# Kernel tuning notes

Hardware: AMD Instinct MI355X
Metric: run time of the kernel (lower is better)

## Reference

```python
import jax, jax.numpy as jnp
import numpy as np

HEAD_DIM = 64

def setup_inputs() -> dict:
    key = jax.random.key(0)
    ks = jax.random.split(key, 6)
    b, q_len, kv_len, emb, h, d = 4, 2048, 2048, 1024, 16, HEAD_DIM
    scale = 1.0 / np.sqrt(emb)  # fan_in variance scaling for stable logits
    return {
        "inputs_q": jax.random.normal(ks[0], (b, q_len, emb), jnp.float32),
        "inputs_kv": jax.random.normal(ks[1], (b, kv_len, emb), jnp.float32),
        "Wq": jax.random.normal(ks[2], (emb, h, d), jnp.float32) * scale,
        "Wk": jax.random.normal(ks[3], (emb, h, d), jnp.float32) * scale,
        "Wv": jax.random.normal(ks[4], (emb, h, d), jnp.float32) * scale,
        "Wo": jax.random.normal(ks[5], (h, d, emb), jnp.float32) * scale,
    }

def reference(inputs_q, inputs_kv, Wq, Wk, Wv, Wo):
    # QKV projections; query kernel init includes 1/sqrt(head_dim) in the
    depth_scale = jnp.sqrt(jnp.asarray(HEAD_DIM, inputs_q.dtype))
    q = jnp.einsum('bqe,ehd->bqhd', inputs_q, Wq) / depth_scale
    k = jnp.einsum('bke,ehd->bkhd', inputs_kv, Wk)
    v = jnp.einsum('bke,ehd->bkhd', inputs_kv, Wv)
    # full attention: einsum -> softmax -> einsum (naive, materializes bhqk)
    attn_weights = jnp.einsum('bqhd,bkhd->bhqk', q, k)
    attn_weights = jax.nn.softmax(attn_weights, axis=-1)
    out = jnp.einsum('bhqk,bkhd->bqhd', attn_weights, v)
    # output projection over (heads, head_dim)
    return jnp.einsum('bqhd,hde->bqe', out, Wo)
```

## Files before the change

### kernel.cpp

```cpp
#include <hip/hip_runtime.h>
#include <hip/hip_bf16.h>


typedef __attribute__((ext_vector_type(8))) short bf16x8;
typedef __attribute__((ext_vector_type(2))) float f32x2;
typedef __attribute__((ext_vector_type(4))) float f32x4;
typedef __attribute__((ext_vector_type(16))) float f32x16;

#define MFMA16(a, b, c) __builtin_amdgcn_mfma_f32_16x16x32_bf16((a), (b), (c), 0, 0, 0)
#define MFMA32(a, b, c) __builtin_amdgcn_mfma_f32_32x32x16_bf16((a), (b), (c), 0, 0, 0)

__device__ __forceinline__ short f2bf(float f) {
  union { float f; unsigned u; } v; v.f = f;
  unsigned r = v.u + 0x7fffu + ((v.u >> 16) & 1u);
  return (short)(r >> 16);
}

__device__ __forceinline__ unsigned cvtpk(float lo, float hi) {
  unsigned r;
  asm("v_cvt_pk_bf16_f32 %0, %1, %2" : "=v"(r) : "v"(lo), "v"(hi));
  return r;
}

__device__ __forceinline__ void plswap(unsigned& a, unsigned& b) {
  asm volatile("v_permlane32_swap_b32 %0, %1" : "+v"(a), "+v"(b));
}

#if __has_builtin(__builtin_amdgcn_permlane32_swap)
typedef __attribute__((ext_vector_type(2))) unsigned u32x2;
__device__ __forceinline__ float xhalf_max(float x) {
  float y = x;
  asm("" : "+v"(y));
  const u32x2 r = __builtin_amdgcn_permlane32_swap(
      __float_as_uint(x), __float_as_uint(y), false, false);
  return fmaxf(__uint_as_float(r[0]), __uint_as_float(r[1]));
}
__device__ __forceinline__ float xhalf_add(float x) {
  float y = x;
  asm("" : "+v"(y));
  const u32x2 r = __builtin_amdgcn_permlane32_swap(
      __float_as_uint(x), __float_as_uint(y), false, false);
  return __uint_as_float(r[0]) + __uint_as_float(r[1]);
}
#else
__device__ __forceinline__ float xhalf_max(float x) {
  float a, b;
  asm volatile(
      "v_mov_b32 %0, %2\n\t"
      "v_mov_b32 %1, %2\n\t"
      "s_nop 2\n\t"
      "v_permlane32_swap_b32 %0, %1"
      : "=&v"(a), "=&v"(b)
      : "v"(x));
  return fmaxf(a, b);
}
__device__ __forceinline__ float xhalf_add(float x) {
  float a, b;
  asm volatile(
      "v_mov_b32 %0, %2\n\t"
      "v_mov_b32 %1, %2\n\t"
      "s_nop 2\n\t"
      "v_permlane32_swap_b32 %0, %1"
      : "=&v"(a), "=&v"(b)
      : "v"(x));
  return a + b;
}
#endif

__device__ __forceinline__ void gld16(const short* g, short* l) {
  __builtin_amdgcn_global_load_lds(
      (const __attribute__((address_space(1))) unsigned int*)g,
      (__attribute__((address_space(3))) unsigned int*)l, 16, 0, 0);
}

__global__ __launch_bounds__(256) void cast_kernel(
    const float* __restrict__ in, short* __restrict__ out, int n8) {
  int i = blockIdx.x * 256 + threadIdx.x;
  const int stride = gridDim.x * 256;
  for (; i < n8; i += stride) {
    const float4 f0 = ((const float4*)in)[2 * i];
    const float4 f1 = ((const float4*)in)[2 * i + 1];
    bf16x8 v;
    v[0] = f2bf(f0.x); v[1] = f2bf(f0.y); v[2] = f2bf(f0.z); v[3] = f2bf(f0.w);
    v[4] = f2bf(f1.x); v[5] = f2bf(f1.y); v[6] = f2bf(f1.z); v[7] = f2bf(f1.w);
    ((bf16x8*)out)[i] = v;
  }
}

__global__ __launch_bounds__(256) void wtrans_kernel(
    const float* __restrict__ w0, const float* __restrict__ w1,
    const float* __restrict__ w2, const float* __restrict__ w3,
    short* __restrict__ out) {
  __shared__ float t[32][33];
  const int z = blockIdx.z;
  const float* src = (z == 0) ? w0 : (z == 1) ? w1 : (z == 2) ? w2 : w3;
  short* dst = out + (size_t)z * (1024 * 1024);
  const int x = threadIdx.x & 31, y = threadIdx.x >> 5;
  const int n0 = blockIdx.x * 32, k0 = blockIdx.y * 32;
#pragma unroll
  for (int yy = y; yy < 32; yy += 8)
    t[yy][x] = src[(size_t)(k0 + yy) * 1024 + n0 + x];
  __syncthreads();
#pragma unroll
  for (int yy = y; yy < 32; yy += 8)
    dst[(size_t)(n0 + yy) * 1024 + k0 + x] = f2bf(t[x][yy]);
}

template <bool OUTF32, bool SWZ>
__global__ __launch_bounds__(256) void gemm_bb(
    const short* __restrict__ A, const short* __restrict__ B,
    void* __restrict__ Cp, int M, int N, int K, int ldc, float scale) {
  __shared__ __align__(16) short At[128][64];
  __shared__ __align__(16) short Bt[128][64];
  const int tid = threadIdx.x, l = tid & 63, w = tid >> 6;
  const int wm = (w >> 1) * 64, wn = (w & 1) * 64;
  int bx = blockIdx.x, by = blockIdx.y;
  if (SWZ) {
    const int nbx = gridDim.x;
    const int lin = by * nbx + bx;
    const int cpx = (nbx * gridDim.y) >> 3;
    const int swz = (lin & 7) * cpx + (lin >> 3);
    bx = swz % nbx;
    by = swz / nbx;
  }
  const int m0 = by * 128, n0 = bx * 128;
  const short* Abase = A + (size_t)(m0 + w * 8 + (l >> 3)) * K + (l & 7) * 8;
  const short* Bbase = B + (size_t)(n0 + w * 8 + (l >> 3)) * K + (l & 7) * 8;

  f32x4 acc[4][4];
#pragma unroll
  for (int i = 0; i < 4; ++i)
#pragma unroll
    for (int j = 0; j < 4; ++j) acc[i][j] = (f32x4){0.f, 0.f, 0.f, 0.f};

  for (int k0 = 0; k0 < K; k0 += 64) {
    __syncthreads();
#pragma unroll
    for (int i = 0; i < 4; ++i) {
      gld16(Abase + (size_t)i * 32 * K + k0, &At[i * 32 + w * 8][0]);
      gld16(Bbase + (size_t)i * 32 * K + k0, &Bt[i * 32 + w * 8][0]);
    }
    __syncthreads();
#pragma unroll
    for (int ks = 0; ks < 2; ++ks) {
      bf16x8 af[4], bfr[4];
#pragma unroll
      for (int mt = 0; mt < 4; ++mt)
        af[mt] = *(const bf16x8*)&At[wm + mt * 16 + (l & 15)][ks * 32 + (l >> 4) * 8];
#pragma unroll
      for (int nt = 0; nt < 4; ++nt)
        bfr[nt] = *(const bf16x8*)&Bt[wn + nt * 16 + (l & 15)][ks * 32 + (l >> 4) * 8];
#pragma unroll
      for (int mt = 0; mt < 4; ++mt)
#pragma unroll
        for (int nt = 0; nt < 4; ++nt)
          acc[mt][nt] = MFMA16(af[mt], bfr[nt], acc[mt][nt]);
    }
  }
#pragma unroll
  for (int mt = 0; mt < 4; ++mt)
#pragma unroll
    for (int nt = 0; nt < 4; ++nt)
#pragma unroll
      for (int r = 0; r < 4; ++r) {
        const int row = m0 + wm + mt * 16 + (l >> 4) * 4 + r;
        const int col = n0 + wn + nt * 16 + (l & 15);
        const float v = acc[mt][nt][r] * scale;
        if (OUTF32)
          ((float*)Cp)[(size_t)row * ldc + col] = v;
        else
          ((short*)Cp)[(size_t)row * ldc + col] = f2bf(v);
      }
}

__global__ __launch_bounds__(512) void attn8w_kernel(
    const short* __restrict__ qb, const short* __restrict__ kb,
    const short* __restrict__ vT, short* __restrict__ ob) {
  __shared__ __align__(16) short Ksh[2][64][64];
  __shared__ __align__(16) short Vsh[2][64][64];
  const int tid = threadIdx.x, w = tid >> 6, l = tid & 63;
  const int hi = l >> 5, ln = l & 31;
  const int lin = blockIdx.y * 8 + blockIdx.x;
  const int swz = (lin & 7) * 64 + (lin >> 3);
  const int qc = swz & 7, bh = swz >> 3;
  const int b = bh >> 4, h = bh & 15;
  const size_t bL = (size_t)b * 2048;
  const int hd = h * 64;
  const int q0 = qc * 256 + w * 32;

  const int sr0 = w * 8 + (l >> 3);
  const int sc0 = ((l & 7) ^ (sr0 & 7)) << 3;

#define STAGE(BUF, KV0)                                                    \
  do {                                                                     \
    gld16(kb + (bL + (KV0) + sr0) * 1024 + hd + sc0, &Ksh[BUF][w * 8][0]); \
    gld16(vT + (size_t)(hd + sr0) * 8192 + bL + (KV0) + sc0,               \
          &Vsh[BUF][w * 8][0]);                                            \
  } while (0)

  bf16x8 qf[4];
  {
    const short* qrow = qb + (bL + q0 + ln) * 1024 + hd + hi * 8;
#pragma unroll
    for (int c = 0; c < 4; ++c) qf[c] = *(const bf16x8*)(qrow + c * 16);
  }

  f32x16 o0, o1;
#pragma unroll
  for (int i = 0; i < 16; ++i) { o0[i] = 0.f; o1[i] = 0.f; }
  float m = -1e30f, lsum = 0.f;

  const int swzk = ln & 7;

  STAGE(0, 0);
  int cur = 0;
  for (int t = 0; t < 32; ++t) {
    __syncthreads();
    if (t < 31) STAGE(cur ^ 1, (t + 1) * 64);

    f32x16 s0, s1;
#pragma unroll
    for (int i = 0; i < 16; ++i) { s0[i] = 0.f; s1[i] = 0.f; }
    __builtin_amdgcn_s_setprio(1);
#pragma unroll
    for (int c = 0; c < 4; ++c) {
      const int bcol = ((((c << 1) | hi)) ^ swzk) << 3;
      const bf16x8 kf0 = *(const bf16x8*)&Ksh[cur][ln][bcol];
      const bf16x8 kf1 = *(const bf16x8*)&Ksh[cur][32 + ln][bcol];
      s0 = MFMA32(kf0, qf[c], s0);
      s1 = MFMA32(kf1, qf[c], s1);
    }
    __builtin_amdgcn_s_setprio(0);

    f32x2 pm0 = (f32x2){s0[0], s0[1]};
    f32x2 pm1 = (f32x2){s1[0], s1[1]};
#pragma unroll
    for (int i = 1; i < 8; ++i) {
      pm0 = __builtin_elementwise_max(pm0, (f32x2){s0[2 * i], s0[2 * i + 1]});
      pm1 = __builtin_elementwise_max(pm1, (f32x2){s1[2 * i], s1[2 * i + 1]});
    }
    pm0 = __builtin_elementwise_max(pm0, pm1);
    float pmax = fmaxf(pm0[0], pm0[1]);
    pmax = xhalf_max(pmax);

    if (!__all(pmax - m <= 8.0f)) {
      const float mnew = fmaxf(m, pmax);
      const float fac = exp2f(m - mnew);
      m = mnew;
      lsum *= fac;
      o0 *= fac;
      o1 *= fac;
    }

    float p0[16], p1[16];
    const f32x2 m2 = (f32x2){m, m};
    f32x2 acc2 = (f32x2){0.f, 0.f};
#pragma unroll
    for (int i = 0; i < 8; ++i) {
      const f32x2 d0 = (f32x2){s0[2 * i], s0[2 * i + 1]} - m2;
      const f32x2 d1 = (f32x2){s1[2 * i], s1[2 * i + 1]} - m2;
      p0[2 * i] = exp2f(d0[0]);
      p0[2 * i + 1] = exp2f(d0[1]);
      p1[2 * i] = exp2f(d1[0]);
      p1[2 * i + 1] = exp2f(d1[1]);
      acc2 += (f32x2){p0[2 * i], p0[2 * i + 1]};
      acc2 += (f32x2){p1[2 * i], p1[2 * i + 1]};
    }
    lsum += acc2[0] + acc2[1];

    __builtin_amdgcn_s_setprio(1);
#define PVCHUNK(PARR, BASE, C)                                               \
  do {                                                                       \
    unsigned A0 = cvtpk(PARR[(BASE) + 0], PARR[(BASE) + 1]);                 \
    unsigned A1 = cvtpk(PARR[(BASE) + 2], PARR[(BASE) + 3]);                 \
    unsigned B0 = cvtpk(PARR[(BASE) + 4], PARR[(BASE) + 5]);                 \
    unsigned B1 = cvtpk(PARR[(BASE) + 6], PARR[(BASE) + 7]);                 \
    plswap(A0, B0);                                                          \
    plswap(A1, B1);                                                          \
    union { unsigned u[4]; bf16x8 v; } pf;                                   \
    pf.u[0] = A0; pf.u[1] = A1; pf.u[2] = B0; pf.u[3] = B1;                  \
    const int bcol = ((((C) << 1) | hi) ^ swzk) << 3;                        \
    const bf16x8 vf0 = *(const bf16x8*)&Vsh[cur][ln][bcol];                  \
    const bf16x8 vf1 = *(const bf16x8*)&Vsh[cur][32 + ln][bcol];             \
    o0 = MFMA32(vf0, pf.v, o0);                                              \
    o1 = MFMA32(vf1, pf.v, o1);                                              \
  } while (0)

    PVCHUNK(p0, 0, 0);
    PVCHUNK(p0, 8, 1);
    PVCHUNK(p1, 0, 2);
    PVCHUNK(p1, 8, 3);
#undef PVCHUNK
    __builtin_amdgcn_s_setprio(0);

    cur ^= 1;
  }

  const float inv = 1.0f / xhalf_add(lsum);
  short* orow = ob + (bL + q0 + ln) * 1024 + hd + hi * 4;
#pragma unroll
  for (int g = 0; g < 4; ++g) {
    const unsigned a0 = cvtpk(o0[4 * g + 0] * inv, o0[4 * g + 1] * inv);
    const unsigned a1 = cvtpk(o0[4 * g + 2] * inv, o0[4 * g + 3] * inv);
    *(uint2*)(orow + 8 * g) = make_uint2(a0, a1);
    const unsigned b0 = cvtpk(o1[4 * g + 0] * inv, o1[4 * g + 1] * inv);
    const unsigned b1 = cvtpk(o1[4 * g + 2] * inv, o1[4 * g + 3] * inv);
    *(uint2*)(orow + 32 + 8 * g) = make_uint2(b0, b1);
  }
#undef STAGE
}

extern "C" void kernel_launch(void* const* d_in, const int* in_sizes, int n_in,
                              void* d_out, int out_size, void* d_ws,
                              size_t ws_size, hipStream_t stream) {
  const size_t ML = (size_t)8192 * 1024;
  short* qb = (short*)d_ws;
  short* kb = qb + ML;
  short* vT = kb + ML;
  short* ob = vT + ML;
  short* wT = ob + ML;
  short* WqT = wT;
  short* WkT = wT + (size_t)1024 * 1024;
  short* WvT = wT + (size_t)2 * 1024 * 1024;
  short* WoT = wT + (size_t)3 * 1024 * 1024;
  short* qibf = vT;
  short* kvbf = ob;

  wtrans_kernel<<<dim3(32, 32, 4), 256, 0, stream>>>(
      (const float*)d_in[2], (const float*)d_in[3], (const float*)d_in[4],
      (const float*)d_in[5], wT);

  cast_kernel<<<2048, 256, 0, stream>>>((const float*)d_in[0], qibf,
                                        (int)(ML / 8));
  cast_kernel<<<2048, 256, 0, stream>>>((const float*)d_in[1], kvbf,
                                        (int)(ML / 8));

  gemm_bb<false, true><<<dim3(8, 64), 256, 0, stream>>>(
      qibf, WqT, qb, 8192, 1024, 1024, 1024, 0.125f * 1.44269504f);
  gemm_bb<false, true><<<dim3(8, 64), 256, 0, stream>>>(
      kvbf, WkT, kb, 8192, 1024, 1024, 1024, 1.0f);
  gemm_bb<false, false><<<dim3(64, 8), 256, 0, stream>>>(
      WvT, kvbf, vT, 1024, 8192, 1024, 8192, 1.0f);

  attn8w_kernel<<<dim3(8, 64), 512, 0, stream>>>(qb, kb, vT, ob);

  gemm_bb<true, true><<<dim3(8, 64), 256, 0, stream>>>(
      ob, WoT, d_out, 8192, 1024, 1024, 1024, 1.0f);
}
```

Baseline: 249.3 us.

## Software-pipeline QK and softmax/PV in attention, merge Q/K projection GEMMs

The attention loop is restructured so the QK^T MFMAs for the next KV tile are issued before the softmax and PV of the previous tile. K stays double-buffered, V moves to a triple buffer, and there are two sets of score registers. The Q and K projection GEMMs are merged into a single launch with a swizzled 3D grid, which cuts one launch and fills the device better. Launch bounds now request 4 waves per SIMD. The extra score registers and the occupancy hint may cause spills, and the extra LDS may limit occupancy.

```diff
diff --git a/kernel.cpp b/kernel.cpp
--- a/kernel.cpp
+++ b/kernel.cpp
@@ -46,23 +46,17 @@
 __device__ __forceinline__ float xhalf_max(float x) {
   float a, b;
   asm volatile(
-      "v_mov_b32 %0, %2\n\t"
-      "v_mov_b32 %1, %2\n\t"
-      "s_nop 2\n\t"
+      "v_mov_b32 %0, %2\n\tv_mov_b32 %1, %2\n\ts_nop 2\n\t"
       "v_permlane32_swap_b32 %0, %1"
-      : "=&v"(a), "=&v"(b)
-      : "v"(x));
+      : "=&v"(a), "=&v"(b) : "v"(x));
   return fmaxf(a, b);
 }
 __device__ __forceinline__ float xhalf_add(float x) {
   float a, b;
   asm volatile(
-      "v_mov_b32 %0, %2\n\t"
-      "v_mov_b32 %1, %2\n\t"
-      "s_nop 2\n\t"
+      "v_mov_b32 %0, %2\n\tv_mov_b32 %1, %2\n\ts_nop 2\n\t"
       "v_permlane32_swap_b32 %0, %1"
-      : "=&v"(a), "=&v"(b)
-      : "v"(x));
+      : "=&v"(a), "=&v"(b) : "v"(x));
   return a + b;
 }
 #endif
@@ -106,24 +100,13 @@
     dst[(size_t)(n0 + yy) * 1024 + k0 + x] = f2bf(t[x][yy]);
 }
 
-template <bool OUTF32, bool SWZ>
-__global__ __launch_bounds__(256) void gemm_bb(
+template <bool OUTF32>
+__device__ __forceinline__ void gemm_body(
     const short* __restrict__ A, const short* __restrict__ B,
-    void* __restrict__ Cp, int M, int N, int K, int ldc, float scale) {
-  __shared__ __align__(16) short At[128][64];
-  __shared__ __align__(16) short Bt[128][64];
+    void* __restrict__ Cp, int K, int ldc, float scale, int m0, int n0,
+    short (*At)[64], short (*Bt)[64]) {
   const int tid = threadIdx.x, l = tid & 63, w = tid >> 6;
   const int wm = (w >> 1) * 64, wn = (w & 1) * 64;
-  int bx = blockIdx.x, by = blockIdx.y;
-  if (SWZ) {
-    const int nbx = gridDim.x;
-    const int lin = by * nbx + bx;
-    const int cpx = (nbx * gridDim.y) >> 3;
-    const int swz = (lin & 7) * cpx + (lin >> 3);
-    bx = swz % nbx;
-    by = swz / nbx;
-  }
-  const int m0 = by * 128, n0 = bx * 128;
   const short* Abase = A + (size_t)(m0 + w * 8 + (l >> 3)) * K + (l & 7) * 8;
   const short* Bbase = B + (size_t)(n0 + w * 8 + (l >> 3)) * K + (l & 7) * 8;
 
@@ -173,11 +156,47 @@
       }
 }
 
-__global__ __launch_bounds__(512) void attn8w_kernel(
+template <bool OUTF32, bool SWZ>
+__global__ __launch_bounds__(256) void gemm_bb(
+    const short* __restrict__ A, const short* __restrict__ B,
+    void* __restrict__ Cp, int M, int N, int K, int ldc, float scale) {
+  __shared__ __align__(16) short At[128][64];
+  __shared__ __align__(16) short Bt[128][64];
+  int bx = blockIdx.x, by = blockIdx.y;
+  if (SWZ) {
+    const int nbx = gridDim.x;
+    const int lin = by * nbx + bx;
+    const int cpx = (nbx * gridDim.y) >> 3;
+    const int swz = (lin & 7) * cpx + (lin >> 3);
+    bx = swz % nbx;
+    by = swz / nbx;
+  }
+  gemm_body<OUTF32>(A, B, Cp, K, ldc, scale, by * 128, bx * 128, At, Bt);
+}
+
+__global__ __launch_bounds__(256) void gemm_qk(
+    const short* __restrict__ Aq, const short* __restrict__ Ak,
+    const short* __restrict__ Bq, const short* __restrict__ Bk,
+    short* __restrict__ Cq, short* __restrict__ Ck, float scaleq) {
+  __shared__ __align__(16) short At[128][64];
+  __shared__ __align__(16) short Bt[128][64];
+  const int lin = (blockIdx.z * 64 + blockIdx.y) * 8 + blockIdx.x;
+  const int swz = (lin & 7) * 128 + (lin >> 3);
+  const int bz = swz >> 9;
+  const int rem = swz & 511;
+  const int by = rem >> 3, bx = rem & 7;
+  const short* A = bz ? Ak : Aq;
+  const short* B = bz ? Bk : Bq;
+  short* C = bz ? Ck : Cq;
+  const float scale = bz ? 1.0f : scaleq;
+  gemm_body<false>(A, B, C, 1024, 1024, scale, by * 128, bx * 128, At, Bt);
+}
+
+__global__ __launch_bounds__(512, 4) void attn8w_kernel(
     const short* __restrict__ qb, const short* __restrict__ kb,
     const short* __restrict__ vT, short* __restrict__ ob) {
   __shared__ __align__(16) short Ksh[2][64][64];
-  __shared__ __align__(16) short Vsh[2][64][64];
+  __shared__ __align__(16) short Vsh[3][64][64];
   const int tid = threadIdx.x, w = tid >> 6, l = tid & 63;
   const int hi = l >> 5, ln = l & 31;
   const int lin = blockIdx.y * 8 + blockIdx.x;
@@ -190,13 +209,11 @@
 
   const int sr0 = w * 8 + (l >> 3);
   const int sc0 = ((l & 7) ^ (sr0 & 7)) << 3;
-
-#define STAGE(BUF, KV0)                                                    \
-  do {                                                                     \
-    gld16(kb + (bL + (KV0) + sr0) * 1024 + hd + sc0, &Ksh[BUF][w * 8][0]); \
-    gld16(vT + (size_t)(hd + sr0) * 8192 + bL + (KV0) + sc0,               \
-          &Vsh[BUF][w * 8][0]);                                            \
-  } while (0)
+  const short* kbase = kb + (bL + sr0) * 1024 + hd + sc0;
+  const short* vbase = vT + (size_t)(hd + sr0) * 8192 + bL + sc0;
+
+#define SK(BUF, KV0) gld16(kbase + (size_t)(KV0) * 1024, &Ksh[BUF][w * 8][0])
+#define SV(SLOT, KV0) gld16(vbase + (KV0), &Vsh[SLOT][w * 8][0])
 
   bf16x8 qf[4];
   {
@@ -212,64 +229,22 @@
 
   const int swzk = ln & 7;
 
-  STAGE(0, 0);
-  int cur = 0;
-  for (int t = 0; t < 32; ++t) {
-    __syncthreads();
-    if (t < 31) STAGE(cur ^ 1, (t + 1) * 64);
-
-    f32x16 s0, s1;
-#pragma unroll
-    for (int i = 0; i < 16; ++i) { s0[i] = 0.f; s1[i] = 0.f; }
-    __builtin_amdgcn_s_setprio(1);
-#pragma unroll
-    for (int c = 0; c < 4; ++c) {
-      const int bcol = ((((c << 1) | hi)) ^ swzk) << 3;
-      const bf16x8 kf0 = *(const bf16x8*)&Ksh[cur][ln][bcol];
-      const bf16x8 kf1 = *(const bf16x8*)&Ksh[cur][32 + ln][bcol];
-      s0 = MFMA32(kf0, qf[c], s0);
-      s1 = MFMA32(kf1, qf[c], s1);
-    }
-    __builtin_amdgcn_s_setprio(0);
-
-    f32x2 pm0 = (f32x2){s0[0], s0[1]};
-    f32x2 pm1 = (f32x2){s1[0], s1[1]};
-#pragma unroll
-    for (int i = 1; i < 8; ++i) {
-      pm0 = __builtin_elementwise_max(pm0, (f32x2){s0[2 * i], s0[2 * i + 1]});
-      pm1 = __builtin_elementwise_max(pm1, (f32x2){s1[2 * i], s1[2 * i + 1]});
-    }
-    pm0 = __builtin_elementwise_max(pm0, pm1);
-    float pmax = fmaxf(pm0[0], pm0[1]);
-    pmax = xhalf_max(pmax);
-
-    if (!__all(pmax - m <= 8.0f)) {
-      const float mnew = fmaxf(m, pmax);
-      const float fac = exp2f(m - mnew);
-      m = mnew;
-      lsum *= fac;
-      o0 *= fac;
-      o1 *= fac;
-    }
-
-    float p0[16], p1[16];
-    const f32x2 m2 = (f32x2){m, m};
-    f32x2 acc2 = (f32x2){0.f, 0.f};
-#pragma unroll
-    for (int i = 0; i < 8; ++i) {
-      const f32x2 d0 = (f32x2){s0[2 * i], s0[2 * i + 1]} - m2;
-      const f32x2 d1 = (f32x2){s1[2 * i], s1[2 * i + 1]} - m2;
-      p0[2 * i] = exp2f(d0[0]);
-      p0[2 * i + 1] = exp2f(d0[1]);
-      p1[2 * i] = exp2f(d1[0]);
-      p1[2 * i + 1] = exp2f(d1[1]);
-      acc2 += (f32x2){p0[2 * i], p0[2 * i + 1]};
-      acc2 += (f32x2){p1[2 * i], p1[2 * i + 1]};
-    }
-    lsum += acc2[0] + acc2[1];
-
-    __builtin_amdgcn_s_setprio(1);
-#define PVCHUNK(PARR, BASE, C)                                               \
+#define QK(KSLOT, S0, S1)                                                    \
+  do {                                                                       \
+    const short(*Kt)[64] = Ksh[KSLOT];                                       \
+    _Pragma("unroll") for (int i = 0; i < 16; ++i) { S0[i] = 0.f; S1[i] = 0.f; } \
+    __builtin_amdgcn_s_setprio(1);                                           \
+    _Pragma("unroll") for (int c = 0; c < 4; ++c) {                          \
+      const int bcol = ((((c << 1) | hi)) ^ swzk) << 3;                      \
+      const bf16x8 kf0 = *(const bf16x8*)&Kt[ln][bcol];                      \
+      const bf16x8 kf1 = *(const bf16x8*)&Kt[32 + ln][bcol];                 \
+      S0 = MFMA32(kf0, qf[c], S0);                                           \
+      S1 = MFMA32(kf1, qf[c], S1);                                           \
+    }                                                                        \
+    __builtin_amdgcn_s_setprio(0);                                           \
+  } while (0)
+
+#define PVCHUNK(PARR, BASE, C, Vt)                                           \
   do {                                                                       \
     unsigned A0 = cvtpk(PARR[(BASE) + 0], PARR[(BASE) + 1]);                 \
     unsigned A1 = cvtpk(PARR[(BASE) + 2], PARR[(BASE) + 3]);                 \
@@ -280,21 +255,80 @@
     union { unsigned u[4]; bf16x8 v; } pf;                                   \
     pf.u[0] = A0; pf.u[1] = A1; pf.u[2] = B0; pf.u[3] = B1;                  \
     const int bcol = ((((C) << 1) | hi) ^ swzk) << 3;                        \
-    const bf16x8 vf0 = *(const bf16x8*)&Vsh[cur][ln][bcol];                  \
-    const bf16x8 vf1 = *(const bf16x8*)&Vsh[cur][32 + ln][bcol];             \
+    const bf16x8 vf0 = *(const bf16x8*)&Vt[ln][bcol];                        \
+    const bf16x8 vf1 = *(const bf16x8*)&Vt[32 + ln][bcol];                   \
     o0 = MFMA32(vf0, pf.v, o0);                                              \
     o1 = MFMA32(vf1, pf.v, o1);                                              \
   } while (0)
 
-    PVCHUNK(p0, 0, 0);
-    PVCHUNK(p0, 8, 1);
-    PVCHUNK(p1, 0, 2);
-    PVCHUNK(p1, 8, 3);
-#undef PVCHUNK
-    __builtin_amdgcn_s_setprio(0);
-
-    cur ^= 1;
-  }
+#define SMPV(VSLOT, S0, S1)                                                  \
+  do {                                                                       \
+    const short(*Vt)[64] = Vsh[VSLOT];                                       \
+    f32x2 pm0 = (f32x2){S0[0], S0[1]};                                       \
+    f32x2 pm1 = (f32x2){S1[0], S1[1]};                                       \
+    _Pragma("unroll") for (int i = 1; i < 8; ++i) {                          \
+      pm0 = __builtin_elementwise_max(pm0, (f32x2){S0[2 * i], S0[2 * i + 1]}); \
+      pm1 = __builtin_elementwise_max(pm1, (f32x2){S1[2 * i], S1[2 * i + 1]}); \
+    }                                                                        \
+    pm0 = __builtin_elementwise_max(pm0, pm1);                               \
+    float pmax = fmaxf(pm0[0], pm0[1]);                                      \
+    pmax = xhalf_max(pmax);                                                  \
+    if (!__all(pmax - m <= 8.0f)) {                                          \
+      const float mnew = fmaxf(m, pmax);                                     \
+      const float fac = exp2f(m - mnew);                                     \
+      m = mnew;                                                              \
+      lsum *= fac;                                                           \
+      o0 *= fac;                                                             \
+      o1 *= fac;                                                             \
+    }                                                                        \
+    float p0[16], p1[16];                                                    \
+    const f32x2 m2 = (f32x2){m, m};                                          \
+    f32x2 acc2 = (f32x2){0.f, 0.f};                                          \
+    _Pragma("unroll") for (int i = 0; i < 8; ++i) {                          \
+      const f32x2 d0 = (f32x2){S0[2 * i], S0[2 * i + 1]} - m2;               \
+      const f32x2 d1 = (f32x2){S1[2 * i], S1[2 * i + 1]} - m2;               \
+      p0[2 * i] = exp2f(d0[0]);                                              \
+      p0[2 * i + 1] = exp2f(d0[1]);                                          \
+      p1[2 * i] = exp2f(d1[0]);                                              \
+      p1[2 * i + 1] = exp2f(d1[1]);                                          \
+      acc2 += (f32x2){p0[2 * i], p0[2 * i + 1]};                             \
+      acc2 += (f32x2){p1[2 * i], p1[2 * i + 1]};                             \
+    }                                                                        \
+    lsum += acc2[0] + acc2[1];                                               \
+    __builtin_amdgcn_s_setprio(1);                                           \
+    PVCHUNK(p0, 0, 0, Vt);                                                   \
+    PVCHUNK(p0, 8, 1, Vt);                                                   \
+    PVCHUNK(p1, 0, 2, Vt);                                                   \
+    PVCHUNK(p1, 8, 3, Vt);                                                   \
+    __builtin_amdgcn_s_setprio(0);                                           \
+  } while (0)
+
+  f32x16 pA0, pA1, pB0, pB1;
+
+  SK(0, 0);
+  SV(0, 0);
+  __syncthreads();
+  SK(1, 64);
+  SV(1, 64);
+  QK(0, pA0, pA1);
+
+  for (int t = 1; t < 31; t += 2) {
+    __syncthreads();
+    SK((t + 1) & 1, (t + 1) * 64);
+    SV((t + 1) % 3, (t + 1) * 64);
+    QK(t & 1, pB0, pB1);
+    SMPV((t - 1) % 3, pA0, pA1);
+
+    __syncthreads();
+    SK((t + 2) & 1, (t + 2) * 64);
+    SV((t + 2) % 3, (t + 2) * 64);
+    QK((t + 1) & 1, pA0, pA1);
+    SMPV(t % 3, pB0, pB1);
+  }
+  __syncthreads();
+  QK(1, pB0, pB1);
+  SMPV(0, pA0, pA1);
+  SMPV(1, pB0, pB1);
 
   const float inv = 1.0f / xhalf_add(lsum);
   short* orow = ob + (bL + q0 + ln) * 1024 + hd + hi * 4;
@@ -307,7 +341,11 @@
     const unsigned b1 = cvtpk(o1[4 * g + 2] * inv, o1[4 * g + 3] * inv);
     *(uint2*)(orow + 32 + 8 * g) = make_uint2(b0, b1);
   }
-#undef STAGE
+#undef SMPV
+#undef PVCHUNK
+#undef QK
+#undef SV
+#undef SK
 }
 
 extern "C" void kernel_launch(void* const* d_in, const int* in_sizes, int n_in,
@@ -335,10 +373,8 @@
   cast_kernel<<<2048, 256, 0, stream>>>((const float*)d_in[1], kvbf,
                                         (int)(ML / 8));
 
-  gemm_bb<false, true><<<dim3(8, 64), 256, 0, stream>>>(
-      qibf, WqT, qb, 8192, 1024, 1024, 1024, 0.125f * 1.44269504f);
-  gemm_bb<false, true><<<dim3(8, 64), 256, 0, stream>>>(
-      kvbf, WkT, kb, 8192, 1024, 1024, 1024, 1.0f);
+  gemm_qk<<<dim3(8, 64, 2), 256, 0, stream>>>(
+      qibf, kvbf, WqT, WkT, qb, kb, 0.125f * 1.44269504f);
   gemm_bb<false, false><<<dim3(64, 8), 256, 0, stream>>>(
       WvT, kvbf, vT, 1024, 8192, 1024, 8192, 1.0f);
 
```

Measured after the change: 506.2 us. +103.0%, slower.
